# Kernel tuning notes

Hardware: AMD Instinct MI355X
Metric: run time of the kernel (lower is better)

The kernel has to match this reference:

```python
import jax, jax.numpy as jnp
import numpy as np

B, S, D = 4, 1024, 384
NUM_ITEMS = 16384
NUM_CLUSTERS = 256
MAX_CLUSTER_SIZE = 128  # 16384/256 = 64 real members, padded to 128 with -1
NEG_INF = -1e9


def setup_inputs() -> dict:
    key = jax.random.key(0)
    k1, k2, k3, k4, k5 = jax.random.split(key, 5)
    hidden_states = jax.random.normal(k1, (B, S, D), dtype=jnp.float32)
    item_embeddings = jax.random.normal(k2, (NUM_ITEMS, D), dtype=jnp.float32) * 0.02
    cluster_embeddings = jax.random.normal(k3, (NUM_CLUSTERS, D), dtype=jnp.float32) * 0.02
    targets = jax.random.randint(k4, (B, S), 0, NUM_ITEMS, dtype=jnp.int32)
    item_mask = (jax.random.uniform(k5, (B, S)) < 0.8).astype(jnp.float32)
    # Deterministic round-robin clustering: item i -> cluster i % C, slot i // C
    cluster_assignments = (jnp.arange(NUM_ITEMS, dtype=jnp.int32) % NUM_CLUSTERS)
    ids = (jnp.arange(NUM_CLUSTERS, dtype=jnp.int32)[:, None]
           + NUM_CLUSTERS * jnp.arange(MAX_CLUSTER_SIZE, dtype=jnp.int32)[None, :])
    cluster_indices = jnp.where(ids < NUM_ITEMS, ids, -1)  # [C, M], padded with -1
    in_cluster_id = (jnp.arange(NUM_ITEMS, dtype=jnp.int32) // NUM_CLUSTERS)
    return {
        "hidden_states": hidden_states,
        "item_embeddings": item_embeddings,
        "cluster_embeddings": cluster_embeddings,
        "item_mask": item_mask,
        "targets": targets,
        "cluster_assignments": cluster_assignments,
        "cluster_indices": cluster_indices,
        "in_cluster_id": in_cluster_id,
    }


def reference(hidden_states, item_embeddings, cluster_embeddings, item_mask,
              targets, cluster_assignments, cluster_indices, in_cluster_id):
    # Level 1: cluster logits / log-probs
    cluster_logits = jnp.einsum('bsd,cd->bsc', hidden_states, cluster_embeddings)
    cluster_log_probs = jax.nn.log_softmax(cluster_logits, axis=-1)
    target_cluster_ids = cluster_assignments[targets]                      # [B,S]
    target_cluster_log_prob = jnp.take_along_axis(
        cluster_log_probs, target_cluster_ids[..., None].astype(jnp.int32), axis=-1
    ).squeeze(-1)                                                          # [B,S]

    # Level 2: gather member embeddings of the target cluster, masked softmax
    cluster_members = cluster_indices[target_cluster_ids]                  # [B,S,M]
    member_emb = item_embeddings[jnp.maximum(cluster_members, 0)]          # [B,S,M,D]
    member_logits = jnp.einsum('bsd,bsmd->bsm', hidden_states, member_emb)  # [B,S,M]
    masked_logits = jnp.where(cluster_members != -1, member_logits, NEG_INF)
    member_log_probs = jax.nn.log_softmax(masked_logits, axis=-1)
    target_pos = in_cluster_id[targets]                                    # [B,S]
    target_item_log_prob = jnp.take_along_axis(
        member_log_probs, target_pos[..., None].astype(jnp.int32), axis=-1
    ).squeeze(-1)

    # Combined loss
    loss_per_token = -(target_cluster_log_prob + target_item_log_prob)
    total_loss = jnp.sum(loss_per_token * item_mask) / (jnp.sum(item_mask) + 1e-8)

    cluster_preds = jnp.argmax(cluster_logits, axis=-1)
    cluster_acc = jnp.mean((cluster_preds == target_cluster_ids).astype(jnp.float32))

    dummy_logits = jnp.zeros(hidden_states.shape[:2] + (item_embeddings.shape[0],),
                             dtype=hidden_states.dtype)
    return (dummy_logits, total_loss,
            -jnp.mean(target_cluster_log_prob),
            -jnp.mean(target_item_log_prob),
            cluster_acc)
```

## Files before the change

### kernel.cpp

```cpp
#include <hip/hip_runtime.h>
#include <math.h>

#define Ddim 384
#define D4 96
#define NUM_ITEMS 16384
#define NUM_CLUSTERS 256
#define MCS 128
#define NEG_INF_F (-1e9f)
#define NTOK 4096
#define TPB 8
#define NCB (NTOK / TPB)
#define NFILLB 2048

__device__ __forceinline__ float dot4(const float4& a, const float4& b) {
    return a.x * b.x + a.y * b.y + a.z * b.z + a.w * b.w;
}

__global__ __launch_bounds__(256) void hs_fill(float* __restrict__ dummy_out)
{
    const size_t base = (size_t)blockIdx.x * 256 + threadIdx.x;
    float4 z; z.x = z.y = z.z = z.w = 0.f;
    float4* o4 = reinterpret_cast<float4*>(dummy_out) + base;
    #pragma unroll 8
    for (int i = 0; i < 32; ++i)
        o4[(size_t)i * (NFILLB * 256)] = z;
}

__global__ __launch_bounds__(512, 2) void hs_compute(
    const float* __restrict__ hidden,
    const float* __restrict__ item_emb,
    const float* __restrict__ cluster_emb,
    const float* __restrict__ item_mask,
    const int*   __restrict__ targets,
    const int*   __restrict__ cluster_assign,
    const int*   __restrict__ cluster_idx,
    const int*   __restrict__ in_cluster_id,
    float* __restrict__ ws)
{
    const int cb   = blockIdx.x;
    const int tid  = threadIdx.x;
    const int t0   = cb * TPB;
    const int lane = tid & 63;
    const int wave = tid >> 6;
    const int wq   = wave & 1;
    const int wqt  = wave >> 1;
    const int q    = lane >> 4;
    const int r    = lane & 15;

    __shared__ float clog[TPB][NUM_CLUSTERS];
    __shared__ float mlog[TPB][64];

    const int tw = t0 + wq * 4;
    const float4* h4 = reinterpret_cast<const float4*>(hidden);
    float4 hf[4][6];
    #pragma unroll
    for (int j = 0; j < 4; ++j)
        #pragma unroll
        for (int i = 0; i < 6; ++i)
            hf[j][i] = h4[(size_t)(tw + j) * D4 + i * 16 + r];

    const float4* ce4 = reinterpret_cast<const float4*>(cluster_emb);
    #pragma unroll 2
    for (int it = 0; it < 16; ++it) {
        const int c = wqt * 64 + it * 4 + q;
        float4 ce[6];
        #pragma unroll
        for (int i = 0; i < 6; ++i) ce[i] = ce4[(size_t)c * D4 + i * 16 + r];
        float a0 = 0.f, a1 = 0.f, a2 = 0.f, a3 = 0.f;
        #pragma unroll
        for (int i = 0; i < 6; ++i) {
            a0 += dot4(ce[i], hf[0][i]);
            a1 += dot4(ce[i], hf[1][i]);
            a2 += dot4(ce[i], hf[2][i]);
            a3 += dot4(ce[i], hf[3][i]);
        }
        const bool hi8 = (r & 8) != 0;
        float u  = hi8 ? a1 : a0;
        float uS = hi8 ? a0 : a1;
        u += __shfl_xor(uS, 8);
        float w  = hi8 ? a3 : a2;
        float wS = hi8 ? a2 : a3;
        w += __shfl_xor(wS, 8);
        const bool hi4 = (r & 4) != 0;
        float zv = hi4 ? w : u;
        float zS = hi4 ? u : w;
        zv += __shfl_xor(zS, 4);
        zv += __shfl_xor(zv, 2);
        zv += __shfl_xor(zv, 1);
        if ((r & 3) == 0) {
            const int m = (r >> 2) & 3;
            const int tokj = (m == 1) ? 2 : (m == 2) ? 1 : m;
            clog[wq * 4 + tokj][c] = zv;
        }
    }
    __syncthreads();

    const int r8 = lane & 7;
    const int g8 = lane >> 3;
    const float4* ie4 = reinterpret_cast<const float4*>(item_emb);

    const int t  = wave;
    const int gt = t0 + t;
    const int tgt  = targets[gt];
    const int tc   = cluster_assign[tgt];
    const int tpos = in_cluster_id[tgt];
    const float msk = item_mask[gt];

    const float v0 = clog[t][lane];
    const float v1 = clog[t][lane + 64];
    const float v2 = clog[t][lane + 128];
    const float v3 = clog[t][lane + 192];
    float bv = v0; int bi = lane;
    if (v1 > bv) { bv = v1; bi = lane + 64;  }
    if (v2 > bv) { bv = v2; bi = lane + 128; }
    if (v3 > bv) { bv = v3; bi = lane + 192; }
    #pragma unroll
    for (int m = 32; m > 0; m >>= 1) {
        const float ov = __shfl_xor(bv, m);
        const int   oi = __shfl_xor(bi, m);
        if (ov > bv || (ov == bv && oi < bi)) { bv = ov; bi = oi; }
    }
    float e = expf(v0 - bv) + expf(v1 - bv) + expf(v2 - bv) + expf(v3 - bv);
    #pragma unroll
    for (int m = 32; m > 0; m >>= 1) e += __shfl_xor(e, m);
    const float lse = bv + logf(e);
    const float tlpc = clog[t][tc] - lse;

    float4 hme[12];
    #pragma unroll
    for (int i = 0; i < 12; ++i)
        hme[i] = h4[(size_t)gt * D4 + i * 8 + r8];
    const int* crow = cluster_idx + (size_t)tc * MCS;
    #pragma unroll 2
    for (int it = 0; it < 8; ++it) {
        const int id = crow[it * 8 + g8];
        const float4* ir = ie4 + (size_t)id * D4;
        float pa = 0.f;
        #pragma unroll
        for (int i = 0; i < 12; ++i) pa += dot4(ir[i * 8 + r8], hme[i]);
        pa += __shfl_xor(pa, 1);
        pa += __shfl_xor(pa, 2);
        pa += __shfl_xor(pa, 4);
        if (r8 == 0) mlog[t][it * 8 + g8] = pa;
    }
    const float w0 = mlog[t][lane];
    float mx = w0;
    #pragma unroll
    for (int m = 32; m > 0; m >>= 1) mx = fmaxf(mx, __shfl_xor(mx, m));
    float e2 = expf(w0 - mx);
    #pragma unroll
    for (int m = 32; m > 0; m >>= 1) e2 += __shfl_xor(e2, m);
    const float tlpi = mlog[t][tpos] - (mx + logf(e2));

    if (lane == 0) {
        ws[NTOK + gt]     = msk;
        ws[2 * NTOK + gt] = tlpc;
        ws[3 * NTOK + gt] = tlpi;
        ws[4 * NTOK + gt] = (bi == tc) ? 1.f : 0.f;
    }
}

__global__ __launch_bounds__(1024) void hs_final(
    const float* __restrict__ ws, float* __restrict__ out)
{
    __shared__ double red[5][1024];
    const int tid = threadIdx.x;
    double a0 = 0, a1 = 0, a2 = 0, a3 = 0, a4 = 0;
    for (int i = tid; i < NTOK; i += 1024) {
        const float msk  = ws[NTOK + i];
        const float tlpc = ws[2 * NTOK + i];
        const float tlpi = ws[3 * NTOK + i];
        a0 += (double)(-(tlpc + tlpi) * msk);
        a1 += (double)msk;
        a2 += (double)tlpc;
        a3 += (double)tlpi;
        a4 += (double)ws[4 * NTOK + i];
    }
    red[0][tid] = a0; red[1][tid] = a1; red[2][tid] = a2;
    red[3][tid] = a3; red[4][tid] = a4;
    __syncthreads();
    for (int s2 = 512; s2 > 0; s2 >>= 1) {
        if (tid < s2) {
            red[0][tid] += red[0][tid + s2];
            red[1][tid] += red[1][tid + s2];
            red[2][tid] += red[2][tid + s2];
            red[3][tid] += red[3][tid + s2];
            red[4][tid] += red[4][tid + s2];
        }
        __syncthreads();
    }
    if (tid == 0) {
        out[0] = (float)(red[0][0] / (red[1][0] + 1e-8));
        out[1] = (float)(-red[2][0] / (double)NTOK);
        out[2] = (float)(-red[3][0] / (double)NTOK);
        out[3] = (float)(red[4][0] / (double)NTOK);
    }
}

extern "C" void kernel_launch(void* const* d_in, const int* in_sizes, int n_in,
                              void* d_out, int out_size, void* d_ws, size_t ws_size,
                              hipStream_t stream) {
    const float* hidden         = (const float*)d_in[0];
    const float* item_emb       = (const float*)d_in[1];
    const float* cluster_emb    = (const float*)d_in[2];
    const float* item_mask      = (const float*)d_in[3];
    const int*   targets        = (const int*)d_in[4];
    const int*   cluster_assign = (const int*)d_in[5];
    const int*   cluster_idx    = (const int*)d_in[6];
    const int*   in_cluster_id  = (const int*)d_in[7];

    float* out = (float*)d_out;
    float* ws  = (float*)d_ws;

    const size_t dummy_elems = (size_t)NTOK * NUM_ITEMS;

    hs_fill<<<NFILLB, 256, 0, stream>>>(out);
    hs_compute<<<NCB, 512, 0, stream>>>(
        hidden, item_emb, cluster_emb, item_mask, targets,
        cluster_assign, cluster_idx, in_cluster_id, ws);
    hs_final<<<1, 1024, 0, stream>>>(ws, out + dummy_elems);
}
```

Before: 116.9 us.

## Sort tokens by target cluster so blocks share gathered item embeddings

An extra block in the fill kernel histograms target clusters, prefix-scans the counts and builds a permutation of token ids grouped by cluster. The compute kernel then handles tokens in that order, so tokens in the same block tend to gather the same cluster's member embeddings, which should improve cache reuse. The cost is one serial counting/scan block, an extra indirection load per token, and non-contiguous reads of hidden rows. The atomic-based scatter order is nondeterministic, but that does not change any result.

```diff
diff --git a/kernel.cpp b/kernel.cpp
--- a/kernel.cpp
+++ b/kernel.cpp
@@ -16,9 +16,47 @@
     return a.x * b.x + a.y * b.y + a.z * b.z + a.w * b.w;
 }
 
-__global__ __launch_bounds__(256) void hs_fill(float* __restrict__ dummy_out)
+__global__ __launch_bounds__(256) void hs_fill_meta(
+    const int* __restrict__ targets, const int* __restrict__ cluster_assign,
+    float* __restrict__ dummy_out, int* __restrict__ wsI)
 {
-    const size_t base = (size_t)blockIdx.x * 256 + threadIdx.x;
+    const int tid = threadIdx.x;
+
+    if (blockIdx.x == NFILLB) {
+        __shared__ int cnt[NUM_CLUSTERS], scan[NUM_CLUSTERS], cur[NUM_CLUSTERS];
+        cnt[tid] = 0; cur[tid] = 0;
+        __syncthreads();
+        int tcv[NTOK / 256];
+        #pragma unroll
+        for (int i = 0; i < NTOK / 256; ++i) {
+            const int t = i * 256 + tid;
+            const int tc = cluster_assign[targets[t]];
+            tcv[i] = tc;
+            atomicAdd(&cnt[tc], 1);
+        }
+        __syncthreads();
+        scan[tid] = cnt[tid];
+        __syncthreads();
+        for (int d = 1; d < 256; d <<= 1) {
+            const int v = (tid >= d) ? scan[tid - d] : 0;
+            __syncthreads();
+            scan[tid] += v;
+            __syncthreads();
+        }
+        wsI[tid] = scan[tid] - cnt[tid];
+        if (tid == 255) wsI[256] = NTOK;
+        __syncthreads();
+        #pragma unroll
+        for (int i = 0; i < NTOK / 256; ++i) {
+            const int t = i * 256 + tid;
+            const int tc = tcv[i];
+            const int p = atomicAdd(&cur[tc], 1);
+            wsI[257 + (scan[tc] - cnt[tc]) + p] = t;
+        }
+        return;
+    }
+
+    const size_t base = (size_t)blockIdx.x * 256 + tid;
     float4 z; z.x = z.y = z.z = z.w = 0.f;
     float4* o4 = reinterpret_cast<float4*>(dummy_out) + base;
     #pragma unroll 8
@@ -35,6 +73,7 @@
     const int*   __restrict__ cluster_assign,
     const int*   __restrict__ cluster_idx,
     const int*   __restrict__ in_cluster_id,
+    const int*   __restrict__ wsI,
     float* __restrict__ ws)
 {
     const int cb   = blockIdx.x;
@@ -50,14 +89,18 @@
     __shared__ float clog[TPB][NUM_CLUSTERS];
     __shared__ float mlog[TPB][64];
 
-    const int tw = t0 + wq * 4;
+    const int* list = wsI + 257;
+
     const float4* h4 = reinterpret_cast<const float4*>(hidden);
+    int tok[4];
+    #pragma unroll
+    for (int j = 0; j < 4; ++j) tok[j] = list[t0 + wq * 4 + j];
     float4 hf[4][6];
     #pragma unroll
     for (int j = 0; j < 4; ++j)
         #pragma unroll
         for (int i = 0; i < 6; ++i)
-            hf[j][i] = h4[(size_t)(tw + j) * D4 + i * 16 + r];
+            hf[j][i] = h4[(size_t)tok[j] * D4 + i * 16 + r];
 
     const float4* ce4 = reinterpret_cast<const float4*>(cluster_emb);
     #pragma unroll 2
@@ -100,7 +143,7 @@
     const float4* ie4 = reinterpret_cast<const float4*>(item_emb);
 
     const int t  = wave;
-    const int gt = t0 + t;
+    const int gt = list[t0 + t];
     const int tgt  = targets[gt];
     const int tc   = cluster_assign[tgt];
     const int tpos = in_cluster_id[tgt];
@@ -211,12 +254,14 @@
 
     float* out = (float*)d_out;
     float* ws  = (float*)d_ws;
+    int*   wsI = (int*)(ws + 5 * NTOK);
 
     const size_t dummy_elems = (size_t)NTOK * NUM_ITEMS;
 
-    hs_fill<<<NFILLB, 256, 0, stream>>>(out);
+    hs_fill_meta<<<NFILLB + 1, 256, 0, stream>>>(
+        targets, cluster_assign, out, wsI);
     hs_compute<<<NCB, 512, 0, stream>>>(
         hidden, item_emb, cluster_emb, item_mask, targets,
-        cluster_assign, cluster_idx, in_cluster_id, ws);
+        cluster_assign, cluster_idx, in_cluster_id, wsI, ws);
     hs_final<<<1, 1024, 0, stream>>>(ws, out + dummy_elems);
 }
```

Measured after the change: 108.2 us (median of 2 runs). 7.5% less time.
